# Performance work log

Hardware: AMD Instinct MI355X
Metric: run time of the kernel (lower is better)

Reference implementation:

```python
import jax, jax.numpy as jnp
import numpy as np

N = 50000   # num nodes
E = 800000  # num edges (avg degree 16)
D = 64      # input feature dim
H = 64      # hidden dim
O = 32      # output dim


def setup_inputs() -> dict:
    key = jax.random.key(0)
    ks = jax.random.split(key, 8)
    def lin(k, fan_in, fan_out):
        # Kaiming-uniform-ish init, stored as [in, out] so forward is x @ W
        bound = 1.0 / np.sqrt(fan_in)
        return jax.random.uniform(k, (fan_in, fan_out), jnp.float32, -bound, bound)
    return {
        "x": jax.random.normal(ks[0], (N, D), jnp.float32),
        "edge_index": jax.random.randint(ks[1], (2, E), 0, N),
        "W_in1": lin(ks[2], D, H),
        "W_neigh1": lin(ks[3], D, H),
        "bias1": jnp.zeros((H,), jnp.float32),
        "W_in2": lin(ks[4], H, H),
        "W_neigh2": lin(ks[5], H, H),
        "bias2": jnp.zeros((H,), jnp.float32),
        "W_out": lin(ks[6], H, O),
        "b_out": jnp.zeros((O,), jnp.float32),
    }


def reference(x, edge_index, W_in1, W_neigh1, bias1, W_in2, W_neigh2, bias2, W_out, b_out):
    row, col = edge_index[0], edge_index[1]  # source, target
    # get_laplacian(sym) + remove_self_loops + negate -> norm = d^-1/2[row] * d^-1/2[col]
    deg = jax.ops.segment_sum(jnp.ones((E,), x.dtype), row, num_segments=N)
    dinv = jnp.where(deg > 0, deg ** -0.5, jnp.zeros((), x.dtype))
    norm = dinv[row] * dinv[col]  # [E]

    def conv(h, W_in, W_neigh, bias):
        # message: gather transformed source features, scale by per-edge norm
        msg = (h @ W_neigh)[row] * norm[:, None]          # [E, out]
        agg = jax.ops.segment_sum(msg, col, num_segments=N)  # scatter-add -> [N, out]
        return h @ W_in + agg + bias[None, :]

    h = jax.nn.relu(conv(x, W_in1, W_neigh1, bias1))
    h = jax.nn.relu(conv(h, W_in2, W_neigh2, bias2))
    return h @ W_out + b_out[None, :]  # variant='equi': per-node output [N, O]
```

## Files before the change

### kernel.cpp

```cpp
#include <hip/hip_runtime.h>
#include <hip/hip_bf16.h>


#define NCHUNK 32
#define NRANGE_H 4
#define HIST_H 12544
#define NRANGE_B 4
#define HIST_B2 12544

typedef __attribute__((ext_vector_type(8))) short bfrag;
typedef __attribute__((ext_vector_type(4))) float f32x4;

__global__ __launch_bounds__(1024) void k_hist(const int* __restrict__ ei,
                                               int* __restrict__ partial,
                                               int N, int E, int range) {
  __shared__ int hist[HIST_H];
  int c = blockIdx.x % NCHUNK;
  int r = (blockIdx.x / NCHUNK) % NRANGE_H;
  int a = blockIdx.x / (NCHUNK * NRANGE_H);
  const int* ids = ei + (size_t)a * E;
  int lo = r * range;
  int hi = min(N, lo + range);
  int len = hi - lo;
  for (int i = threadIdx.x; i < len; i += 1024) hist[i] = 0;
  __syncthreads();
  int e0 = (int)((long long)E * c / NCHUNK);
  int e1 = (int)((long long)E * (c + 1) / NCHUNK);
  for (int e = e0 + threadIdx.x; e < e1; e += 1024) {
    int id = ids[e];
    if (id >= lo && id < hi) atomicAdd(&hist[id - lo], 1);
  }
  __syncthreads();
  int* dst = partial + ((size_t)a * NCHUNK + c) * N + lo;
  for (int i = threadIdx.x; i < len; i += 1024) dst[i] = hist[i];
}

__global__ __launch_bounds__(1024) void k_dinv_scan(const int* __restrict__ partial,
                                                    float* __restrict__ dinv,
                                                    int* __restrict__ indeg,
                                                    int* __restrict__ ptr,
                                                    int* __restrict__ bsum, int N) {
  __shared__ int s[1024];
  int g = blockIdx.x * 1024 + threadIdx.x;
  int deg = 0, ind = 0;
  if (g < N) {
#pragma unroll
    for (int c = 0; c < NCHUNK; ++c) {
      deg += partial[(size_t)c * N + g];
      ind += partial[((size_t)NCHUNK + c) * N + g];
    }
    dinv[g] = (deg > 0) ? (1.0f / sqrtf((float)deg)) : 0.0f;
    indeg[g] = ind;
  }
  s[threadIdx.x] = ind;
  __syncthreads();
  for (int off = 1; off < 1024; off <<= 1) {
    int tv = (threadIdx.x >= off) ? s[threadIdx.x - off] : 0;
    __syncthreads();
    s[threadIdx.x] += tv;
    __syncthreads();
  }
  if (g < N) ptr[g] = s[threadIdx.x] - ind;
  if (threadIdx.x == 1023) bsum[blockIdx.x] = s[1023];
}

__global__ __launch_bounds__(256) void k_base(const int* __restrict__ partial,
                                              const int* __restrict__ bsum,
                                              int* __restrict__ ptr,
                                              int* __restrict__ base, int N, int nb) {
  __shared__ int pbs[64];
  if (threadIdx.x == 0) {
    int acc = 0;
    for (int i = 0; i < nb; ++i) { pbs[i] = acc; acc += bsum[i]; }
  }
  __syncthreads();
  int n = blockIdx.x * 256 + threadIdx.x;
  if (n >= N) return;
  int run = ptr[n] + pbs[n >> 10];
  ptr[n] = run;
#pragma unroll
  for (int c = 0; c < NCHUNK; ++c) {
    base[(size_t)c * N + n] = run;
    run += partial[((size_t)NCHUNK + c) * N + n];
  }
}

__global__ __launch_bounds__(1024) void k_bin2(const int* __restrict__ ei,
                                               const int* __restrict__ base,
                                               int* __restrict__ csr_row,
                                               int N, int E, int range) {
  __shared__ int cnt[HIST_B2];
  int c = blockIdx.x % NCHUNK;
  int r = blockIdx.x / NCHUNK;
  const int* row = ei;
  const int* col = ei + E;
  int lo = r * range;
  int hi = min(N, lo + range);
  int len = hi - lo;
  for (int i = threadIdx.x; i < len; i += 1024) cnt[i] = 0;
  __syncthreads();
  int e0 = (int)((long long)E * c / NCHUNK);
  int e1 = (int)((long long)E * (c + 1) / NCHUNK);
  const int* bslice = base + (size_t)c * N;
  for (int e = e0 + threadIdx.x; e < e1; e += 1024) {
    int cl = col[e];
    int rw = row[e];
    if (cl >= lo && cl < hi) {
      int off = atomicAdd(&cnt[cl - lo], 1);
      csr_row[bslice[cl] + off] = rw;
    }
  }
}

template <bool RELU>
__global__ __launch_bounds__(256) void k_dual_gemm_mfma(
    const float* h,
    const float* __restrict__ Wn,
    const float* __restrict__ Wi,
    const float* __restrict__ bias,
    const float* __restrict__ dinv,
    __hip_bfloat16* __restrict__ t, float* agg, int N) {
  __shared__ short Wn_f[4096];
  __shared__ short Wi_f[4096];
  __shared__ float b_s[64];

  const int tid = threadIdx.x;
  for (int i = tid; i < 4096; i += 256) {
    int k = i >> 6, n = i & 63;
    int dst = (((n >> 4) * 2 + (k >> 5)) * 64 + ((k >> 3) & 3) * 16 + (n & 15)) * 8 + (k & 7);
    __hip_bfloat16 a = __float2bfloat16(Wn[i]);
    __hip_bfloat16 b = __float2bfloat16(Wi[i]);
    Wn_f[dst] = *(short*)&a;
    Wi_f[dst] = *(short*)&b;
  }
  if (tid < 64) b_s[tid] = bias[tid];
  __syncthreads();

  const int lane = tid & 63;
  const int w = tid >> 6;
  const int m = lane & 15;
  const int quad = lane >> 4;

  bfrag Bn[4][2], Bi[4][2];
#pragma unroll
  for (int ct = 0; ct < 4; ++ct)
#pragma unroll
    for (int kb = 0; kb < 2; ++kb) {
      Bn[ct][kb] = *(const bfrag*)&Wn_f[((ct * 2 + kb) * 64 + lane) * 8];
      Bi[ct][kb] = *(const bfrag*)&Wi_f[((ct * 2 + kb) * 64 + lane) * 8];
    }

  const int r0 = blockIdx.x * 64 + w * 16;
  const int arow = r0 + m;

  bfrag A[2];
#pragma unroll
  for (int kb = 0; kb < 2; ++kb) {
    bfrag av = {};
    if (arow < N) {
      const float* src = &h[(size_t)arow * 64 + kb * 32 + quad * 8];
      float4 f0 = *(const float4*)src;
      float4 f1 = *(const float4*)(src + 4);
      float tmp[8] = {f0.x, f0.y, f0.z, f0.w, f1.x, f1.y, f1.z, f1.w};
#pragma unroll
      for (int j = 0; j < 8; ++j) {
        float v = RELU ? fmaxf(tmp[j], 0.f) : tmp[j];
        __hip_bfloat16 hb = __float2bfloat16(v);
        av[j] = *(short*)&hb;
      }
    }
    A[kb] = av;
  }

  f32x4 accT[4], accA[4];
#pragma unroll
  for (int ct = 0; ct < 4; ++ct) {
    f32x4 z = {0.f, 0.f, 0.f, 0.f};
    accT[ct] = z;
    accA[ct] = z;
  }
#pragma unroll
  for (int ct = 0; ct < 4; ++ct) {
    accT[ct] = __builtin_amdgcn_mfma_f32_16x16x32_bf16(A[0], Bn[ct][0], accT[ct], 0, 0, 0);
    accT[ct] = __builtin_amdgcn_mfma_f32_16x16x32_bf16(A[1], Bn[ct][1], accT[ct], 0, 0, 0);
    accA[ct] = __builtin_amdgcn_mfma_f32_16x16x32_bf16(A[0], Bi[ct][0], accA[ct], 0, 0, 0);
    accA[ct] = __builtin_amdgcn_mfma_f32_16x16x32_bf16(A[1], Bi[ct][1], accA[ct], 0, 0, 0);
  }

#pragma unroll
  for (int reg = 0; reg < 4; ++reg) {
    int r = r0 + quad * 4 + reg;
    if (r < N) {
      float dv = dinv[r];
#pragma unroll
      for (int ct = 0; ct < 4; ++ct) {
        int col = ct * 16 + m;
        t[(size_t)r * 64 + col] = __float2bfloat16(accT[ct][reg] * dv);
        agg[(size_t)r * 64 + col] = accA[ct][reg] + b_s[col];
      }
    }
  }
}

__global__ __launch_bounds__(256) void k_gather(
    const int* __restrict__ csr_row, const int* __restrict__ ptr,
    const int* __restrict__ indeg, const float* __restrict__ dinv,
    const __hip_bfloat16* __restrict__ t, float* __restrict__ agg, int N) {
  int n = blockIdx.x * 4 + (threadIdx.x >> 6);
  if (n >= N) return;
  int lane = threadIdx.x & 63;
  int q = lane >> 4;
  int fl = lane & 15;
  int i0 = ptr[n];
  int end = i0 + indeg[n];
  float dn = dinv[n];

  float4 aggv = make_float4(0.f, 0.f, 0.f, 0.f);
  if (q == 0) aggv = *(const float4*)&agg[(size_t)n * 64 + 4 * fl];

  float4 acc = make_float4(0.f, 0.f, 0.f, 0.f);
  int i = i0 + q;
  for (; i + 4 < end; i += 8) {
    int ra = csr_row[i];
    int rb = csr_row[i + 4];
    ushort4 ua = *(const ushort4*)&t[(size_t)ra * 64 + 4 * fl];
    ushort4 ub = *(const ushort4*)&t[(size_t)rb * 64 + 4 * fl];
    float4 va, vb;
    ((unsigned*)&va)[0] = (unsigned)ua.x << 16; ((unsigned*)&va)[1] = (unsigned)ua.y << 16;
    ((unsigned*)&va)[2] = (unsigned)ua.z << 16; ((unsigned*)&va)[3] = (unsigned)ua.w << 16;
    ((unsigned*)&vb)[0] = (unsigned)ub.x << 16; ((unsigned*)&vb)[1] = (unsigned)ub.y << 16;
    ((unsigned*)&vb)[2] = (unsigned)ub.z << 16; ((unsigned*)&vb)[3] = (unsigned)ub.w << 16;
    acc.x += va.x + vb.x; acc.y += va.y + vb.y;
    acc.z += va.z + vb.z; acc.w += va.w + vb.w;
  }
  for (; i < end; i += 4) {
    int ra = csr_row[i];
    ushort4 ua = *(const ushort4*)&t[(size_t)ra * 64 + 4 * fl];
    float4 va;
    ((unsigned*)&va)[0] = (unsigned)ua.x << 16; ((unsigned*)&va)[1] = (unsigned)ua.y << 16;
    ((unsigned*)&va)[2] = (unsigned)ua.z << 16; ((unsigned*)&va)[3] = (unsigned)ua.w << 16;
    acc.x += va.x; acc.y += va.y; acc.z += va.z; acc.w += va.w;
  }
  acc.x += __shfl_xor(acc.x, 16); acc.y += __shfl_xor(acc.y, 16);
  acc.z += __shfl_xor(acc.z, 16); acc.w += __shfl_xor(acc.w, 16);
  acc.x += __shfl_xor(acc.x, 32); acc.y += __shfl_xor(acc.y, 32);
  acc.z += __shfl_xor(acc.z, 32); acc.w += __shfl_xor(acc.w, 32);
  if (q == 0) {
    aggv.x += dn * acc.x; aggv.y += dn * acc.y;
    aggv.z += dn * acc.z; aggv.w += dn * acc.w;
    *(float4*)&agg[(size_t)n * 64 + 4 * fl] = aggv;
  }
}

__global__ __launch_bounds__(256) void k_gather_out(
    const int* __restrict__ csr_row, const int* __restrict__ ptr,
    const int* __restrict__ indeg, const float* __restrict__ dinv,
    const __hip_bfloat16* __restrict__ t, const float* __restrict__ agg,
    const float* __restrict__ Wo,
    const float* __restrict__ bo,
    float* __restrict__ out, int N) {
  __shared__ float Wo_s[64 * 32];
  __shared__ float bo_s[32];
  __shared__ float rowbuf[4][64];

  const int tid = threadIdx.x;
  for (int i = tid; i < 2048; i += 256) Wo_s[i] = Wo[i];
  if (tid < 32) bo_s[tid] = bo[tid];
  __syncthreads();

  int w = tid >> 6;
  int n = blockIdx.x * 4 + w;
  if (n >= N) return;
  int lane = tid & 63;
  int q = lane >> 4;
  int fl = lane & 15;
  int i0 = ptr[n];
  int end = i0 + indeg[n];
  float dn = dinv[n];

  float4 aggv = make_float4(0.f, 0.f, 0.f, 0.f);
  if (q == 0) aggv = *(const float4*)&agg[(size_t)n * 64 + 4 * fl];

  float4 acc = make_float4(0.f, 0.f, 0.f, 0.f);
  int i = i0 + q;
  for (; i + 4 < end; i += 8) {
    int ra = csr_row[i];
    int rb = csr_row[i + 4];
    ushort4 ua = *(const ushort4*)&t[(size_t)ra * 64 + 4 * fl];
    ushort4 ub = *(const ushort4*)&t[(size_t)rb * 64 + 4 * fl];
    float4 va, vb;
    ((unsigned*)&va)[0] = (unsigned)ua.x << 16; ((unsigned*)&va)[1] = (unsigned)ua.y << 16;
    ((unsigned*)&va)[2] = (unsigned)ua.z << 16; ((unsigned*)&va)[3] = (unsigned)ua.w << 16;
    ((unsigned*)&vb)[0] = (unsigned)ub.x << 16; ((unsigned*)&vb)[1] = (unsigned)ub.y << 16;
    ((unsigned*)&vb)[2] = (unsigned)ub.z << 16; ((unsigned*)&vb)[3] = (unsigned)ub.w << 16;
    acc.x += va.x + vb.x; acc.y += va.y + vb.y;
    acc.z += va.z + vb.z; acc.w += va.w + vb.w;
  }
  for (; i < end; i += 4) {
    int ra = csr_row[i];
    ushort4 ua = *(const ushort4*)&t[(size_t)ra * 64 + 4 * fl];
    float4 va;
    ((unsigned*)&va)[0] = (unsigned)ua.x << 16; ((unsigned*)&va)[1] = (unsigned)ua.y << 16;
    ((unsigned*)&va)[2] = (unsigned)ua.z << 16; ((unsigned*)&va)[3] = (unsigned)ua.w << 16;
    acc.x += va.x; acc.y += va.y; acc.z += va.z; acc.w += va.w;
  }
  acc.x += __shfl_xor(acc.x, 16); acc.y += __shfl_xor(acc.y, 16);
  acc.z += __shfl_xor(acc.z, 16); acc.w += __shfl_xor(acc.w, 16);
  acc.x += __shfl_xor(acc.x, 32); acc.y += __shfl_xor(acc.y, 32);
  acc.z += __shfl_xor(acc.z, 32); acc.w += __shfl_xor(acc.w, 32);
  if (q == 0) {
    rowbuf[w][4 * fl + 0] = fmaxf(aggv.x + dn * acc.x, 0.f);
    rowbuf[w][4 * fl + 1] = fmaxf(aggv.y + dn * acc.y, 0.f);
    rowbuf[w][4 * fl + 2] = fmaxf(aggv.z + dn * acc.z, 0.f);
    rowbuf[w][4 * fl + 3] = fmaxf(aggv.w + dn * acc.w, 0.f);
  }
  int half = lane >> 5;
  int j = lane & 31;
  float ov = 0.f;
#pragma unroll 8
  for (int k = 32 * half; k < 32 * half + 32; ++k)
    ov = fmaf(rowbuf[w][k], Wo_s[k * 32 + j], ov);
  ov += __shfl_xor(ov, 32);
  if (half == 0) out[(size_t)n * 32 + j] = ov + bo_s[j];
}

extern "C" void kernel_launch(void* const* d_in, const int* in_sizes, int n_in,
                              void* d_out, int out_size, void* d_ws, size_t ws_size,
                              hipStream_t stream) {
  const float* x = (const float*)d_in[0];
  const int* ei = (const int*)d_in[1];
  const float* W_in1 = (const float*)d_in[2];
  const float* W_neigh1 = (const float*)d_in[3];
  const float* bias1 = (const float*)d_in[4];
  const float* W_in2 = (const float*)d_in[5];
  const float* W_neigh2 = (const float*)d_in[6];
  const float* bias2 = (const float*)d_in[7];
  const float* W_out = (const float*)d_in[8];
  const float* b_out = (const float*)d_in[9];
  float* out = (float*)d_out;

  const int N = in_sizes[0] / 64;
  const int E = in_sizes[1] / 2;

  char* ws = (char*)d_ws;
  size_t off = 0;
  auto alloc = [&](size_t bytes) -> void* {
    void* p = ws + off;
    off += (bytes + 255) & ~(size_t)255;
    return p;
  };
  float* dinv = (float*)alloc((size_t)N * 4);
  int* indeg = (int*)alloc((size_t)N * 4);
  int* ptr = (int*)alloc((size_t)N * 4);
  int* bsum = (int*)alloc(256);
  int* csr_row = (int*)alloc((size_t)E * 4);
  int* partial = (int*)alloc((size_t)2 * NCHUNK * N * 4);
  int* base = (int*)alloc((size_t)NCHUNK * N * 4);
  __hip_bfloat16* t = (__hip_bfloat16*)alloc((size_t)N * 64 * 2);
  float* agg = (float*)alloc((size_t)N * 64 * 4);
  (void)ws_size;

  int range_h = (N + NRANGE_H - 1) / NRANGE_H;
  int range_b = (N + NRANGE_B - 1) / NRANGE_B;
  int gN = (N + 255) / 256;
  int gRows = (N + 63) / 64;
  int gNode = (N + 3) / 4;
  int nb = (N + 1023) / 1024;

  k_hist<<<2 * NRANGE_H * NCHUNK, 1024, 0, stream>>>(ei, partial, N, E, range_h);
  k_dinv_scan<<<nb, 1024, 0, stream>>>(partial, dinv, indeg, ptr, bsum, N);
  k_base<<<gN, 256, 0, stream>>>(partial, bsum, ptr, base, N, nb);
  k_bin2<<<NRANGE_B * NCHUNK, 1024, 0, stream>>>(ei, base, csr_row, N, E, range_b);

  k_dual_gemm_mfma<false><<<gRows, 256, 0, stream>>>(x, W_neigh1, W_in1, bias1, dinv, t, agg, N);
  k_gather<<<gNode, 256, 0, stream>>>(csr_row, ptr, indeg, dinv, t, agg, N);

  k_dual_gemm_mfma<true><<<gRows, 256, 0, stream>>>(agg, W_neigh2, W_in2, bias2, dinv, t, agg, N);
  k_gather_out<<<gNode, 256, 0, stream>>>(csr_row, ptr, indeg, dinv, t, agg,
                                          W_out, b_out, out, N);
}
```

Measured before the change: 203.1 us.

## Fuse layer-1 dual GEMM into histogram kernel by moving dinv scaling to gather

The first-layer dual GEMM no longer depends on dinv, so it runs inside the histogram launch as extra blocks, removing one kernel launch and letting the GEMM overlap with the degree histogram. To allow this, the layer-1 gather now multiplies each neighbor's bf16 feature by dinv[src] per edge instead of using a pre-scaled t. This adds a per-edge dinv load and FMA work in the gather, and the fused kernel uses 1024-thread blocks with large shared memory for the GEMM part.

```diff
diff --git a/kernel.cpp b/kernel.cpp
--- a/kernel.cpp
+++ b/kernel.cpp
@@ -11,28 +11,132 @@
 typedef __attribute__((ext_vector_type(8))) short bfrag;
 typedef __attribute__((ext_vector_type(4))) float f32x4;
 
-__global__ __launch_bounds__(1024) void k_hist(const int* __restrict__ ei,
-                                               int* __restrict__ partial,
-                                               int N, int E, int range) {
-  __shared__ int hist[HIST_H];
-  int c = blockIdx.x % NCHUNK;
-  int r = (blockIdx.x / NCHUNK) % NRANGE_H;
-  int a = blockIdx.x / (NCHUNK * NRANGE_H);
+template <bool RELU, bool PRESCALE>
+__device__ __forceinline__ void gemm_tile16(
+    const float* h, const float* __restrict__ dinv,
+    const short* Wn_f, const short* Wi_f, const float* b_s,
+    __hip_bfloat16* __restrict__ t, float* agg, int r0, int lane, int N) {
+  const int m = lane & 15;
+  const int quad = lane >> 4;
+
+  bfrag Bn[4][2], Bi[4][2];
+#pragma unroll
+  for (int ct = 0; ct < 4; ++ct)
+#pragma unroll
+    for (int kb = 0; kb < 2; ++kb) {
+      Bn[ct][kb] = *(const bfrag*)&Wn_f[((ct * 2 + kb) * 64 + lane) * 8];
+      Bi[ct][kb] = *(const bfrag*)&Wi_f[((ct * 2 + kb) * 64 + lane) * 8];
+    }
+
+  const int arow = r0 + m;
+  bfrag A[2];
+#pragma unroll
+  for (int kb = 0; kb < 2; ++kb) {
+    bfrag av = {};
+    if (arow < N) {
+      const float* src = &h[(size_t)arow * 64 + kb * 32 + quad * 8];
+      float4 f0 = *(const float4*)src;
+      float4 f1 = *(const float4*)(src + 4);
+      float tmp[8] = {f0.x, f0.y, f0.z, f0.w, f1.x, f1.y, f1.z, f1.w};
+#pragma unroll
+      for (int j = 0; j < 8; ++j) {
+        float v = RELU ? fmaxf(tmp[j], 0.f) : tmp[j];
+        __hip_bfloat16 hb = __float2bfloat16(v);
+        av[j] = *(short*)&hb;
+      }
+    }
+    A[kb] = av;
+  }
+
+  f32x4 accT[4], accA[4];
+#pragma unroll
+  for (int ct = 0; ct < 4; ++ct) {
+    f32x4 z = {0.f, 0.f, 0.f, 0.f};
+    accT[ct] = z;
+    accA[ct] = z;
+  }
+#pragma unroll
+  for (int ct = 0; ct < 4; ++ct) {
+    accT[ct] = __builtin_amdgcn_mfma_f32_16x16x32_bf16(A[0], Bn[ct][0], accT[ct], 0, 0, 0);
+    accT[ct] = __builtin_amdgcn_mfma_f32_16x16x32_bf16(A[1], Bn[ct][1], accT[ct], 0, 0, 0);
+    accA[ct] = __builtin_amdgcn_mfma_f32_16x16x32_bf16(A[0], Bi[ct][0], accA[ct], 0, 0, 0);
+    accA[ct] = __builtin_amdgcn_mfma_f32_16x16x32_bf16(A[1], Bi[ct][1], accA[ct], 0, 0, 0);
+  }
+
+#pragma unroll
+  for (int reg = 0; reg < 4; ++reg) {
+    int r = r0 + quad * 4 + reg;
+    if (r < N) {
+      float dv = PRESCALE ? dinv[r] : 1.0f;
+#pragma unroll
+      for (int ct = 0; ct < 4; ++ct) {
+        int col = ct * 16 + m;
+        float tv = PRESCALE ? accT[ct][reg] * dv : accT[ct][reg];
+        t[(size_t)r * 64 + col] = __float2bfloat16(tv);
+        agg[(size_t)r * 64 + col] = accA[ct][reg] + b_s[col];
+      }
+    }
+  }
+}
+
+__device__ __forceinline__ void stage_W_frag(const float* __restrict__ Wn,
+                                             const float* __restrict__ Wi,
+                                             short* Wn_f, short* Wi_f,
+                                             int tid, int nthr) {
+  for (int i = tid; i < 4096; i += nthr) {
+    int k = i >> 6, n = i & 63;
+    int dst = (((n >> 4) * 2 + (k >> 5)) * 64 + ((k >> 3) & 3) * 16 + (n & 15)) * 8 + (k & 7);
+    __hip_bfloat16 a = __float2bfloat16(Wn[i]);
+    __hip_bfloat16 b = __float2bfloat16(Wi[i]);
+    Wn_f[dst] = *(short*)&a;
+    Wi_f[dst] = *(short*)&b;
+  }
+}
+
+__global__ __launch_bounds__(1024) void k_hist_gemm1(
+    const int* __restrict__ ei, int* __restrict__ partial,
+    const float* __restrict__ x,
+    const float* __restrict__ Wn, const float* __restrict__ Wi,
+    const float* __restrict__ bias,
+    __hip_bfloat16* __restrict__ t, float* __restrict__ agg,
+    int N, int E, int range, int gemmBlocks) {
+  __shared__ __align__(16) char smem[HIST_H * 4];
+  const int tid = threadIdx.x;
+
+  if ((int)blockIdx.x < gemmBlocks) {
+    short* Wn_f = (short*)smem;
+    short* Wi_f = (short*)(smem + 8192);
+    float* b_s = (float*)(smem + 16384);
+    stage_W_frag(Wn, Wi, Wn_f, Wi_f, tid, 1024);
+    if (tid < 64) b_s[tid] = bias[tid];
+    __syncthreads();
+    int w = tid >> 6;
+    int lane = tid & 63;
+    int r0 = blockIdx.x * 256 + w * 16;
+    gemm_tile16<false, false>(x, nullptr, Wn_f, Wi_f, b_s, t, agg, r0, lane, N);
+    return;
+  }
+
+  int* hist = (int*)smem;
+  int bid = blockIdx.x - gemmBlocks;
+  int c = bid % NCHUNK;
+  int r = (bid / NCHUNK) % NRANGE_H;
+  int a = bid / (NCHUNK * NRANGE_H);
   const int* ids = ei + (size_t)a * E;
   int lo = r * range;
   int hi = min(N, lo + range);
   int len = hi - lo;
-  for (int i = threadIdx.x; i < len; i += 1024) hist[i] = 0;
+  for (int i = tid; i < len; i += 1024) hist[i] = 0;
   __syncthreads();
   int e0 = (int)((long long)E * c / NCHUNK);
   int e1 = (int)((long long)E * (c + 1) / NCHUNK);
-  for (int e = e0 + threadIdx.x; e < e1; e += 1024) {
+  for (int e = e0 + tid; e < e1; e += 1024) {
     int id = ids[e];
     if (id >= lo && id < hi) atomicAdd(&hist[id - lo], 1);
   }
   __syncthreads();
   int* dst = partial + ((size_t)a * NCHUNK + c) * N + lo;
-  for (int i = threadIdx.x; i < len; i += 1024) dst[i] = hist[i];
+  for (int i = tid; i < len; i += 1024) dst[i] = hist[i];
 }
 
 __global__ __launch_bounds__(1024) void k_dinv_scan(const int* __restrict__ partial,
@@ -112,8 +216,7 @@
   }
 }
 
-template <bool RELU>
-__global__ __launch_bounds__(256) void k_dual_gemm_mfma(
+__global__ __launch_bounds__(256) void k_dual_gemm2(
     const float* h,
     const float* __restrict__ Wn,
     const float* __restrict__ Wi,
@@ -123,83 +226,14 @@
   __shared__ short Wn_f[4096];
   __shared__ short Wi_f[4096];
   __shared__ float b_s[64];
-
   const int tid = threadIdx.x;
-  for (int i = tid; i < 4096; i += 256) {
-    int k = i >> 6, n = i & 63;
-    int dst = (((n >> 4) * 2 + (k >> 5)) * 64 + ((k >> 3) & 3) * 16 + (n & 15)) * 8 + (k & 7);
-    __hip_bfloat16 a = __float2bfloat16(Wn[i]);
-    __hip_bfloat16 b = __float2bfloat16(Wi[i]);
-    Wn_f[dst] = *(short*)&a;
-    Wi_f[dst] = *(short*)&b;
-  }
+  stage_W_frag(Wn, Wi, Wn_f, Wi_f, tid, 256);
   if (tid < 64) b_s[tid] = bias[tid];
   __syncthreads();
-
-  const int lane = tid & 63;
-  const int w = tid >> 6;
-  const int m = lane & 15;
-  const int quad = lane >> 4;
-
-  bfrag Bn[4][2], Bi[4][2];
-#pragma unroll
-  for (int ct = 0; ct < 4; ++ct)
-#pragma unroll
-    for (int kb = 0; kb < 2; ++kb) {
-      Bn[ct][kb] = *(const bfrag*)&Wn_f[((ct * 2 + kb) * 64 + lane) * 8];
-      Bi[ct][kb] = *(const bfrag*)&Wi_f[((ct * 2 + kb) * 64 + lane) * 8];
-    }
-
-  const int r0 = blockIdx.x * 64 + w * 16;
-  const int arow = r0 + m;
-
-  bfrag A[2];
-#pragma unroll
-  for (int kb = 0; kb < 2; ++kb) {
-    bfrag av = {};
-    if (arow < N) {
-      const float* src = &h[(size_t)arow * 64 + kb * 32 + quad * 8];
-      float4 f0 = *(const float4*)src;
-      float4 f1 = *(const float4*)(src + 4);
-      float tmp[8] = {f0.x, f0.y, f0.z, f0.w, f1.x, f1.y, f1.z, f1.w};
-#pragma unroll
-      for (int j = 0; j < 8; ++j) {
-        float v = RELU ? fmaxf(tmp[j], 0.f) : tmp[j];
-        __hip_bfloat16 hb = __float2bfloat16(v);
-        av[j] = *(short*)&hb;
-      }
-    }
-    A[kb] = av;
-  }
-
-  f32x4 accT[4], accA[4];
-#pragma unroll
-  for (int ct = 0; ct < 4; ++ct) {
-    f32x4 z = {0.f, 0.f, 0.f, 0.f};
-    accT[ct] = z;
-    accA[ct] = z;
-  }
-#pragma unroll
-  for (int ct = 0; ct < 4; ++ct) {
-    accT[ct] = __builtin_amdgcn_mfma_f32_16x16x32_bf16(A[0], Bn[ct][0], accT[ct], 0, 0, 0);
-    accT[ct] = __builtin_amdgcn_mfma_f32_16x16x32_bf16(A[1], Bn[ct][1], accT[ct], 0, 0, 0);
-    accA[ct] = __builtin_amdgcn_mfma_f32_16x16x32_bf16(A[0], Bi[ct][0], accA[ct], 0, 0, 0);
-    accA[ct] = __builtin_amdgcn_mfma_f32_16x16x32_bf16(A[1], Bi[ct][1], accA[ct], 0, 0, 0);
-  }
-
-#pragma unroll
-  for (int reg = 0; reg < 4; ++reg) {
-    int r = r0 + quad * 4 + reg;
-    if (r < N) {
-      float dv = dinv[r];
-#pragma unroll
-      for (int ct = 0; ct < 4; ++ct) {
-        int col = ct * 16 + m;
-        t[(size_t)r * 64 + col] = __float2bfloat16(accT[ct][reg] * dv);
-        agg[(size_t)r * 64 + col] = accA[ct][reg] + b_s[col];
-      }
-    }
-  }
+  int w = tid >> 6;
+  int lane = tid & 63;
+  int r0 = blockIdx.x * 64 + w * 16;
+  gemm_tile16<true, true>(h, dinv, Wn_f, Wi_f, b_s, t, agg, r0, lane, N);
 }
 
 __global__ __launch_bounds__(256) void k_gather(
@@ -223,6 +257,8 @@
   for (; i + 4 < end; i += 8) {
     int ra = csr_row[i];
     int rb = csr_row[i + 4];
+    float na = dinv[ra];
+    float nb = dinv[rb];
     ushort4 ua = *(const ushort4*)&t[(size_t)ra * 64 + 4 * fl];
     ushort4 ub = *(const ushort4*)&t[(size_t)rb * 64 + 4 * fl];
     float4 va, vb;
@@ -230,16 +266,20 @@
     ((unsigned*)&va)[2] = (unsigned)ua.z << 16; ((unsigned*)&va)[3] = (unsigned)ua.w << 16;
     ((unsigned*)&vb)[0] = (unsigned)ub.x << 16; ((unsigned*)&vb)[1] = (unsigned)ub.y << 16;
     ((unsigned*)&vb)[2] = (unsigned)ub.z << 16; ((unsigned*)&vb)[3] = (unsigned)ub.w << 16;
-    acc.x += va.x + vb.x; acc.y += va.y + vb.y;
-    acc.z += va.z + vb.z; acc.w += va.w + vb.w;
+    acc.x = fmaf(va.x, na, acc.x); acc.y = fmaf(va.y, na, acc.y);
+    acc.z = fmaf(va.z, na, acc.z); acc.w = fmaf(va.w, na, acc.w);
+    acc.x = fmaf(vb.x, nb, acc.x); acc.y = fmaf(vb.y, nb, acc.y);
+    acc.z = fmaf(vb.z, nb, acc.z); acc.w = fmaf(vb.w, nb, acc.w);
   }
   for (; i < end; i += 4) {
     int ra = csr_row[i];
+    float na = dinv[ra];
     ushort4 ua = *(const ushort4*)&t[(size_t)ra * 64 + 4 * fl];
     float4 va;
     ((unsigned*)&va)[0] = (unsigned)ua.x << 16; ((unsigned*)&va)[1] = (unsigned)ua.y << 16;
     ((unsigned*)&va)[2] = (unsigned)ua.z << 16; ((unsigned*)&va)[3] = (unsigned)ua.w << 16;
-    acc.x += va.x; acc.y += va.y; acc.z += va.z; acc.w += va.w;
+    acc.x = fmaf(va.x, na, acc.x); acc.y = fmaf(va.y, na, acc.y);
+    acc.z = fmaf(va.z, na, acc.z); acc.w = fmaf(va.w, na, acc.w);
   }
   acc.x += __shfl_xor(acc.x, 16); acc.y += __shfl_xor(acc.y, 16);
   acc.z += __shfl_xor(acc.z, 16); acc.w += __shfl_xor(acc.w, 16);
@@ -366,16 +406,17 @@
   int gRows = (N + 63) / 64;
   int gNode = (N + 3) / 4;
   int nb = (N + 1023) / 1024;
-
-  k_hist<<<2 * NRANGE_H * NCHUNK, 1024, 0, stream>>>(ei, partial, N, E, range_h);
+  int gemmBlocks = (N + 255) / 256;
+
+  k_hist_gemm1<<<gemmBlocks + 2 * NRANGE_H * NCHUNK, 1024, 0, stream>>>(
+      ei, partial, x, W_neigh1, W_in1, bias1, t, agg, N, E, range_h, gemmBlocks);
   k_dinv_scan<<<nb, 1024, 0, stream>>>(partial, dinv, indeg, ptr, bsum, N);
   k_base<<<gN, 256, 0, stream>>>(partial, bsum, ptr, base, N, nb);
   k_bin2<<<NRANGE_B * NCHUNK, 1024, 0, stream>>>(ei, base, csr_row, N, E, range_b);
 
-  k_dual_gemm_mfma<false><<<gRows, 256, 0, stream>>>(x, W_neigh1, W_in1, bias1, dinv, t, agg, N);
   k_gather<<<gNode, 256, 0, stream>>>(csr_row, ptr, indeg, dinv, t, agg, N);
 
-  k_dual_gemm_mfma<true><<<gRows, 256, 0, stream>>>(agg, W_neigh2, W_in2, bias2, dinv, t, agg, N);
+  k_dual_gemm2<<<gRows, 256, 0, stream>>>(agg, W_neigh2, W_in2, bias2, dinv, t, agg, N);
   k_gather_out<<<gNode, 256, 0, stream>>>(csr_row, ptr, indeg, dinv, t, agg,
                                           W_out, b_out, out, N);
 }
```

After: 199.4 us, median of 2. About the same (-1.9%).
